# Kernel tuning notes

Measured on AMD Instinct MI355X. Metric: run time of the kernel, lower is better.

## Reference

```python
import jax, jax.numpy as jnp
import numpy as np

N_T = 100  # number of time grid points for the ODE solve, matching torch.linspace(0, 1, 100)


def setup_inputs() -> dict:
    key = jax.random.key(0)
    kx, kw, kb, kc, kd = jax.random.split(key, 5)
    H = 1024
    N = 16384
    return {
        "x": jax.random.normal(kx, (N, H), dtype=jnp.float32),
        "W": jax.random.normal(kw, (H, H), dtype=jnp.float32),
        "b": jax.random.normal(kb, (H,), dtype=jnp.float32),
        "c": jax.random.normal(kc, (H,), dtype=jnp.float32),
        "d": jax.random.normal(kd, (H,), dtype=jnp.float32),
    }


def reference(x, W, b, c, d):
    # fused matmul + trig elementwise: z = x @ W + b*sin(x) + c*cos(x) + d*tan(x)
    z = jnp.matmul(x, W) + b * jnp.sin(x) + c * jnp.cos(x) + d * jnp.tan(x)

    # ODE: dy/dt = -y + t*z, y(0)=0, integrated on linspace(0,1,100), return y(1).
    ts = jnp.linspace(0.0, 1.0, N_T, dtype=z.dtype)
    t0 = ts[:-1]
    dts = ts[1:] - ts[:-1]

    def f(t, y):
        return -y + t * z

    def rk4_step(y, t_dt):
        t, dt = t_dt
        k1 = f(t, y)
        k2 = f(t + 0.5 * dt, y + 0.5 * dt * k1)
        k3 = f(t + 0.5 * dt, y + 0.5 * dt * k2)
        k4 = f(t + dt, y + dt * k3)
        y_next = y + (dt / 6.0) * (k1 + 2.0 * k2 + 2.0 * k3 + k4)
        return y_next, None

    y0 = jnp.zeros_like(z)
    y_final, _ = jax.lax.scan(rk4_step, y0, (t0, dts))
    return y_final
```

## Files before the change

### kernel.cpp

```cpp
#include <hip/hip_runtime.h>
#include <hip/hip_bf16.h>

typedef __attribute__((ext_vector_type(4))) float  f32x4;
typedef __attribute__((ext_vector_type(8))) short  bf16x8;
typedef __attribute__((ext_vector_type(4))) short  bf16x4v;

#define BM 128
#define BN 128
#define BK 64
#define PADK 72
#define EPAD 68
#define SMEM_BYTES 36864

__device__ __forceinline__ unsigned short f2bf(float f) {
  __hip_bfloat16 h = __float2bfloat16(f);
  unsigned short u; __builtin_memcpy(&u, &h, 2); return u;
}

__device__ __forceinline__ void my_sincos(float xf, float& s_out, float& c_out) {
  const double xd = (double)xf;
  const double kd = __builtin_rint(xd * 0.636619772367581343076);
  const int    q  = (int)kd;
  double rd = __builtin_fma(-kd, 1.5707963267948966,    xd);
  rd        = __builtin_fma(-kd, 6.123233995736766e-17, rd);
  const float r = (float)rd;
  const float z = r * r;
  const float ps = fmaf(z, fmaf(z, fmaf(z, 2.7183114939898219e-06f,
                                           -1.9839334836096632e-04f),
                                   8.3333293858894632e-03f),
                        -1.6666666641626524e-01f);
  const float sr = fmaf(r * z, ps, r);
  const float pc = fmaf(z, fmaf(z, fmaf(z, 2.4390448796277409e-05f,
                                           -1.3886763774609929e-03f),
                                   4.1666623323739063e-02f),
                        -4.9999999725103100e-01f);
  const float cr = fmaf(z, pc, 1.0f);
  const bool swap = (q & 1) != 0;
  float s1 = swap ? cr : sr;
  float c1 = swap ? sr : cr;
  if (q & 2)       s1 = -s1;
  if ((q + 1) & 2) c1 = -c1;
  s_out = s1; c_out = c1;
}

__global__ __launch_bounds__(256)
void transpose_W(const float* __restrict__ W, unsigned short* __restrict__ Wt, int H) {
  __shared__ float tile[64][65];
  const int k0 = blockIdx.y * 64;
  const int n0 = blockIdx.x * 64;
  const int t = threadIdx.x;
  #pragma unroll
  for (int it = 0; it < 4; ++it) {
    int q = it * 256 + t;
    int r = q >> 4, c4 = (q & 15) << 2;
    f32x4 v = *(const f32x4*)&W[(size_t)(k0 + r) * H + n0 + c4];
    tile[r][c4 + 0] = v[0]; tile[r][c4 + 1] = v[1];
    tile[r][c4 + 2] = v[2]; tile[r][c4 + 3] = v[3];
  }
  __syncthreads();
  #pragma unroll
  for (int it = 0; it < 4; ++it) {
    int q = it * 256 + t;
    int r = q >> 4, c4 = (q & 15) << 2;
    bf16x4v o;
    #pragma unroll
    for (int j = 0; j < 4; ++j) o[j] = (short)f2bf(tile[c4 + j][r]);
    *(bf16x4v*)&Wt[(size_t)(n0 + r) * H + k0 + c4] = o;
  }
}

__global__ __launch_bounds__(256)
void cvt_x(const float* __restrict__ x, unsigned short* __restrict__ xb, int n4) {
  int i = blockIdx.x * 256 + threadIdx.x;
  const int stride = gridDim.x * 256;
  for (; i < n4; i += stride) {
    f32x4 v = ((const f32x4*)x)[i];
    bf16x4v o;
    #pragma unroll
    for (int j = 0; j < 4; ++j) o[j] = (short)f2bf(v[j]);
    ((bf16x4v*)xb)[i] = o;
  }
}

template <bool XB>
__global__ __launch_bounds__(256, 2)
void gemm_fused(const float* __restrict__ x, const unsigned short* __restrict__ xb,
                const unsigned short* __restrict__ Wt,
                const float* __restrict__ bv, const float* __restrict__ cv,
                const float* __restrict__ dv, float* __restrict__ out,
                float S, int H) {
  __shared__ unsigned char smem[SMEM_BYTES];
  unsigned short* As = (unsigned short*)smem;
  unsigned short* Bs = As + BM * PADK;
  float*          Es = (float*)smem;

  const int tid  = threadIdx.x;
  const int nwg  = gridDim.x;
  const int work = (blockIdx.x & 7) * (nwg >> 3) + (blockIdx.x >> 3);
  const int bj   = work & 7;
  const int bi   = work >> 3;
  const int i0   = bi * BM, j0 = bj * BN;
  const int wave = tid >> 6, lane = tid & 63;
  const int wr = wave >> 1, wc = wave & 1;
  const int l16 = lane & 15, lq = lane >> 4;

  f32x4 acc[4][4] = {};

  for (int kk = 0; kk < H; kk += BK) {
    if constexpr (XB) {
      #pragma unroll
      for (int it = 0; it < 4; ++it) {
        int q = it * 256 + tid;
        int r = q >> 3, c8 = (q & 7) << 3;
        bf16x8 v = *(const bf16x8*)&xb[(size_t)(i0 + r) * H + kk + c8];
        *(bf16x8*)&As[r * PADK + c8] = v;
      }
    } else {
      #pragma unroll
      for (int it = 0; it < 8; ++it) {
        int q = it * 256 + tid;
        int r = q >> 4, c4 = (q & 15) << 2;
        f32x4 v = *(const f32x4*)&x[(size_t)(i0 + r) * H + kk + c4];
        bf16x4v o;
        #pragma unroll
        for (int j = 0; j < 4; ++j) o[j] = (short)f2bf(v[j]);
        *(bf16x4v*)&As[r * PADK + c4] = o;
      }
    }
    #pragma unroll
    for (int it = 0; it < 4; ++it) {
      int q = it * 256 + tid;
      int r = q >> 3, c8 = (q & 7) << 3;
      bf16x8 v = *(const bf16x8*)&Wt[(size_t)(j0 + r) * H + kk + c8];
      *(bf16x8*)&Bs[r * PADK + c8] = v;
    }
    __syncthreads();

    #pragma unroll
    for (int s = 0; s < 2; ++s) {
      bf16x8 af[4], bfr[4];
      #pragma unroll
      for (int mi = 0; mi < 4; ++mi)
        af[mi] = *(const bf16x8*)&As[(wr * 64 + mi * 16 + l16) * PADK + s * 32 + lq * 8];
      #pragma unroll
      for (int ni = 0; ni < 4; ++ni)
        bfr[ni] = *(const bf16x8*)&Bs[(wc * 64 + ni * 16 + l16) * PADK + s * 32 + lq * 8];
      #pragma unroll
      for (int mi = 0; mi < 4; ++mi)
        #pragma unroll
        for (int ni = 0; ni < 4; ++ni)
          acc[mi][ni] = __builtin_amdgcn_mfma_f32_16x16x32_bf16(af[mi], bfr[ni], acc[mi][ni], 0, 0, 0);
    }
    __syncthreads();
  }

  float* ep = Es + wave * (16 * EPAD);
  const int rr = lane >> 2;
  const int cq = (lane & 3) * 16;
  #pragma unroll
  for (int mi = 0; mi < 4; ++mi) {
    #pragma unroll
    for (int ni = 0; ni < 4; ++ni)
      #pragma unroll
      for (int r = 0; r < 4; ++r)
        ep[(lq * 4 + r) * EPAD + ni * 16 + l16] = acc[mi][ni][r];
    const int i  = i0 + wr * 64 + mi * 16 + rr;
    const int jb = j0 + wc * 64 + cq;
    const float* xrow = &x[(size_t)i * H + jb];
    float*       orow = &out[(size_t)i * H + jb];
    #pragma unroll
    for (int t = 0; t < 4; ++t) {
      f32x4 a  = *(const f32x4*)&ep[rr * EPAD + cq + 4 * t];
      f32x4 xv = *(const f32x4*)&xrow[4 * t];
      f32x4 b4 = *(const f32x4*)&bv[jb + 4 * t];
      f32x4 c4 = *(const f32x4*)&cv[jb + 4 * t];
      f32x4 d4 = *(const f32x4*)&dv[jb + 4 * t];
      f32x4 o;
      #pragma unroll
      for (int e = 0; e < 4; ++e) {
        float s, co;
        my_sincos(xv[e], s, co);
        o[e] = S * (a[e] + b4[e] * s + c4[e] * co + d4[e] * (s / co));
      }
      *(f32x4*)&orow[4 * t] = o;
    }
  }
}

extern "C" void kernel_launch(void* const* d_in, const int* in_sizes, int n_in,
                              void* d_out, int out_size, void* d_ws, size_t ws_size,
                              hipStream_t stream) {
  const float* x = (const float*)d_in[0];
  const float* W = (const float*)d_in[1];
  const float* b = (const float*)d_in[2];
  const float* c = (const float*)d_in[3];
  const float* d = (const float*)d_in[4];
  float* out = (float*)d_out;
  const int H = in_sizes[2];
  const int M = in_sizes[0] / H;

  const int NT = 100;
  float ts[NT];
  const float step = (float)(1.0 / 99.0);
  for (int i = 0; i < NT; ++i) ts[i] = (float)i * step;
  ts[NT - 1] = 1.0f;
  double yy = 0.0;
  for (int i = 0; i < NT - 1; ++i) {
    const double t = (double)ts[i], dt = (double)(ts[i + 1] - ts[i]);
    const double k1 = t - yy;
    const double k2 = (t + 0.5 * dt) - (yy + 0.5 * dt * k1);
    const double k3 = (t + 0.5 * dt) - (yy + 0.5 * dt * k2);
    const double k4 = (t + dt) - (yy + dt * k3);
    yy += dt / 6.0 * (k1 + 2.0 * k2 + 2.0 * k3 + k4);
  }
  const float S = (float)yy;

  unsigned short* Wt = (unsigned short*)d_ws;
  dim3 tgrid(H / 64, H / 64);
  transpose_W<<<tgrid, 256, 0, stream>>>(W, Wt, H);

  const size_t need = (size_t)H * H * 2 + (size_t)M * H * 2;
  const int nblk = (H / BN) * (M / BM);

  if (ws_size >= need) {
    unsigned short* xb = Wt + (size_t)H * H;
    cvt_x<<<2048, 256, 0, stream>>>(x, xb, M * H / 4);
    gemm_fused<true><<<nblk, 256, 0, stream>>>(x, xb, Wt, b, c, d, out, S, H);
  } else {
    gemm_fused<false><<<nblk, 256, 0, stream>>>(x, nullptr, Wt, b, c, d, out, S, H);
  }
}
```

Before: 83.91 us.

## Precompute trig term in bf16 during prep pass and fuse prep kernels

Moves the sin/cos/tan elementwise term out of the GEMM epilogue into a combined prep kernel that also transposes W and converts x to bf16, storing the trig sum as a bf16 buffer. The epilogue then just adds this buffer to the accumulator and scales. It also switches range reduction to a float multiply and uses a hardware reciprocal for tan. This trades epilogue ALU work for an extra workspace buffer write/read and bf16 rounding of the trig term.

```diff
diff --git a/kernel.cpp b/kernel.cpp
--- a/kernel.cpp
+++ b/kernel.cpp
@@ -16,12 +16,16 @@
   __hip_bfloat16 h = __float2bfloat16(f);
   unsigned short u; __builtin_memcpy(&u, &h, 2); return u;
 }
+__device__ __forceinline__ float bf2f(short u) {
+  unsigned int w = ((unsigned int)(unsigned short)u) << 16;
+  float f; __builtin_memcpy(&f, &w, 4); return f;
+}
 
 __device__ __forceinline__ void my_sincos(float xf, float& s_out, float& c_out) {
-  const double xd = (double)xf;
-  const double kd = __builtin_rint(xd * 0.636619772367581343076);
-  const int    q  = (int)kd;
-  double rd = __builtin_fma(-kd, 1.5707963267948966,    xd);
+  const float kf = __builtin_rintf(xf * 0.636619772367581343f);
+  const int   q  = (int)kf;
+  const double kd = (double)kf;
+  double rd = __builtin_fma(-kd, 1.5707963267948966,    (double)xf);
   rd        = __builtin_fma(-kd, 6.123233995736766e-17, rd);
   const float r = (float)rd;
   const float z = r * r;
@@ -44,6 +48,61 @@
 }
 
 __global__ __launch_bounds__(256)
+void prep_all(const float* __restrict__ W, const float* __restrict__ x,
+              const float* __restrict__ bv, const float* __restrict__ cv,
+              const float* __restrict__ dv,
+              unsigned short* __restrict__ Wt, unsigned short* __restrict__ xb,
+              unsigned short* __restrict__ g, int H, int n4) {
+  __shared__ float tile[64][65];
+  const int t = threadIdx.x;
+  if (blockIdx.x < 256) {
+    const int blk = blockIdx.x;
+    const int n0 = (blk & 15) << 6;
+    const int k0 = (blk >> 4) << 6;
+    #pragma unroll
+    for (int it = 0; it < 4; ++it) {
+      int q = it * 256 + t;
+      int r = q >> 4, c4 = (q & 15) << 2;
+      f32x4 v = *(const f32x4*)&W[(size_t)(k0 + r) * H + n0 + c4];
+      tile[r][c4 + 0] = v[0]; tile[r][c4 + 1] = v[1];
+      tile[r][c4 + 2] = v[2]; tile[r][c4 + 3] = v[3];
+    }
+    __syncthreads();
+    #pragma unroll
+    for (int it = 0; it < 4; ++it) {
+      int q = it * 256 + t;
+      int r = q >> 4, c4 = (q & 15) << 2;
+      bf16x4v o;
+      #pragma unroll
+      for (int j = 0; j < 4; ++j) o[j] = (short)f2bf(tile[c4 + j][r]);
+      *(bf16x4v*)&Wt[(size_t)(n0 + r) * H + k0 + c4] = o;
+    }
+  } else {
+    const int jm = (H >> 2) - 1;
+    int i = (blockIdx.x - 256) * 256 + t;
+    const int stride = ((int)gridDim.x - 256) * 256;
+    for (; i < n4; i += stride) {
+      f32x4 v = ((const f32x4*)x)[i];
+      const int j4 = (i & jm) << 2;
+      f32x4 b4 = *(const f32x4*)&bv[j4];
+      f32x4 c4 = *(const f32x4*)&cv[j4];
+      f32x4 d4 = *(const f32x4*)&dv[j4];
+      bf16x4v xo, go;
+      #pragma unroll
+      for (int e = 0; e < 4; ++e) {
+        xo[e] = (short)f2bf(v[e]);
+        float s, co;
+        my_sincos(v[e], s, co);
+        const float tn = s * __builtin_amdgcn_rcpf(co);
+        go[e] = (short)f2bf(fmaf(b4[e], s, fmaf(c4[e], co, d4[e] * tn)));
+      }
+      ((bf16x4v*)xb)[i] = xo;
+      ((bf16x4v*)g)[i]  = go;
+    }
+  }
+}
+
+__global__ __launch_bounds__(256)
 void transpose_W(const float* __restrict__ W, unsigned short* __restrict__ Wt, int H) {
   __shared__ float tile[64][65];
   const int k0 = blockIdx.y * 64;
@@ -68,7 +127,6 @@
     *(bf16x4v*)&Wt[(size_t)(n0 + r) * H + k0 + c4] = o;
   }
 }
-
 __global__ __launch_bounds__(256)
 void cvt_x(const float* __restrict__ x, unsigned short* __restrict__ xb, int n4) {
   int i = blockIdx.x * 256 + threadIdx.x;
@@ -82,10 +140,11 @@
   }
 }
 
-template <bool XB>
+template <int MODE>
 __global__ __launch_bounds__(256, 2)
 void gemm_fused(const float* __restrict__ x, const unsigned short* __restrict__ xb,
                 const unsigned short* __restrict__ Wt,
+                const unsigned short* __restrict__ g,
                 const float* __restrict__ bv, const float* __restrict__ cv,
                 const float* __restrict__ dv, float* __restrict__ out,
                 float S, int H) {
@@ -107,7 +166,7 @@
   f32x4 acc[4][4] = {};
 
   for (int kk = 0; kk < H; kk += BK) {
-    if constexpr (XB) {
+    if constexpr (MODE <= 1) {
       #pragma unroll
       for (int it = 0; it < 4; ++it) {
         int q = it * 256 + tid;
@@ -166,23 +225,37 @@
         ep[(lq * 4 + r) * EPAD + ni * 16 + l16] = acc[mi][ni][r];
     const int i  = i0 + wr * 64 + mi * 16 + rr;
     const int jb = j0 + wc * 64 + cq;
-    const float* xrow = &x[(size_t)i * H + jb];
-    float*       orow = &out[(size_t)i * H + jb];
-    #pragma unroll
-    for (int t = 0; t < 4; ++t) {
-      f32x4 a  = *(const f32x4*)&ep[rr * EPAD + cq + 4 * t];
-      f32x4 xv = *(const f32x4*)&xrow[4 * t];
-      f32x4 b4 = *(const f32x4*)&bv[jb + 4 * t];
-      f32x4 c4 = *(const f32x4*)&cv[jb + 4 * t];
-      f32x4 d4 = *(const f32x4*)&dv[jb + 4 * t];
-      f32x4 o;
-      #pragma unroll
-      for (int e = 0; e < 4; ++e) {
-        float s, co;
-        my_sincos(xv[e], s, co);
-        o[e] = S * (a[e] + b4[e] * s + c4[e] * co + d4[e] * (s / co));
-      }
-      *(f32x4*)&orow[4 * t] = o;
+    float* orow = &out[(size_t)i * H + jb];
+    if constexpr (MODE == 0) {
+      const unsigned short* grow = &g[(size_t)i * H + jb];
+      #pragma unroll
+      for (int t = 0; t < 4; ++t) {
+        f32x4 a = *(const f32x4*)&ep[rr * EPAD + cq + 4 * t];
+        bf16x4v gv = *(const bf16x4v*)&grow[4 * t];
+        f32x4 o;
+        #pragma unroll
+        for (int e = 0; e < 4; ++e) o[e] = S * (a[e] + bf2f(gv[e]));
+        *(f32x4*)&orow[4 * t] = o;
+      }
+    } else {
+      const float* xrow = &x[(size_t)i * H + jb];
+      #pragma unroll
+      for (int t = 0; t < 4; ++t) {
+        f32x4 a  = *(const f32x4*)&ep[rr * EPAD + cq + 4 * t];
+        f32x4 xv = *(const f32x4*)&xrow[4 * t];
+        f32x4 b4 = *(const f32x4*)&bv[jb + 4 * t];
+        f32x4 c4 = *(const f32x4*)&cv[jb + 4 * t];
+        f32x4 d4 = *(const f32x4*)&dv[jb + 4 * t];
+        f32x4 o;
+        #pragma unroll
+        for (int e = 0; e < 4; ++e) {
+          float s, co;
+          my_sincos(xv[e], s, co);
+          const float tanv = s * __builtin_amdgcn_rcpf(co);
+          o[e] = S * (fmaf(b4[e], s, a[e]) + fmaf(c4[e], co, d4[e] * tanv));
+        }
+        *(f32x4*)&orow[4 * t] = o;
+      }
     }
   }
 }
@@ -216,17 +289,24 @@
   const float S = (float)yy;
 
   unsigned short* Wt = (unsigned short*)d_ws;
-  dim3 tgrid(H / 64, H / 64);
-  transpose_W<<<tgrid, 256, 0, stream>>>(W, Wt, H);
-
-  const size_t need = (size_t)H * H * 2 + (size_t)M * H * 2;
+  unsigned short* xb = Wt + (size_t)H * H;
+  unsigned short* g  = xb + (size_t)M * H;
+  const size_t needW  = (size_t)H * H * 2;
+  const size_t needXb = (size_t)M * H * 2;
+  const int n4   = M * H / 4;
   const int nblk = (H / BN) * (M / BM);
 
-  if (ws_size >= need) {
-    unsigned short* xb = Wt + (size_t)H * H;
-    cvt_x<<<2048, 256, 0, stream>>>(x, xb, M * H / 4);
-    gemm_fused<true><<<nblk, 256, 0, stream>>>(x, xb, Wt, b, c, d, out, S, H);
+  if (ws_size >= needW + 2 * needXb) {
+    prep_all<<<256 + 2048, 256, 0, stream>>>(W, x, b, c, d, Wt, xb, g, H, n4);
+    gemm_fused<0><<<nblk, 256, 0, stream>>>(x, xb, Wt, g, b, c, d, out, S, H);
+  } else if (ws_size >= needW + needXb) {
+    dim3 tgrid(H / 64, H / 64);
+    transpose_W<<<tgrid, 256, 0, stream>>>(W, Wt, H);
+    cvt_x<<<2048, 256, 0, stream>>>(x, xb, n4);
+    gemm_fused<1><<<nblk, 256, 0, stream>>>(x, xb, Wt, nullptr, b, c, d, out, S, H);
   } else {
-    gemm_fused<false><<<nblk, 256, 0, stream>>>(x, nullptr, Wt, b, c, d, out, S, H);
-  }
-}
+    dim3 tgrid(H / 64, H / 64);
+    transpose_W<<<tgrid, 256, 0, stream>>>(W, Wt, H);
+    gemm_fused<2><<<nblk, 256, 0, stream>>>(x, nullptr, Wt, nullptr, b, c, d, out, S, H);
+  }
+}
```

Result: slower. 85.92 us (+2.4%).
